# Performance work log

Hardware: AMD Instinct MI355X
Metric: run time of the kernel (lower is better)

Reference implementation:

```python
import jax, jax.numpy as jnp
import numpy as np

NUM_SENT, SENT_LEN, HIDDEN, OUT = 128, 64, 512, 512
N = NUM_SENT * SENT_LEN


def setup_inputs() -> dict:
    key = jax.random.key(0)
    ks = jax.random.split(key, 14)
    s = 1.0 / np.sqrt(HIDDEN)
    so = 1.0 / np.sqrt(OUT)
    return {
        "x": jax.random.normal(ks[0], (NUM_SENT, SENT_LEN, HIDDEN), jnp.float32),
        "mask": jax.random.uniform(ks[1], (N,), jnp.float32),
        "a_ud": jax.random.normal(ks[2], (N, N), jnp.float32) * 0.01,
        "a_lr": jax.random.normal(ks[3], (N, N), jnp.float32) * 0.01,
        "W": jax.random.uniform(ks[4], (OUT, HIDDEN), jnp.float32, -s, s),
        "b": jax.random.uniform(ks[5], (OUT,), jnp.float32, -s, s),
        "W_ud": jax.random.uniform(ks[6], (OUT, HIDDEN), jnp.float32, -s, s),
        "b_ud": jax.random.uniform(ks[7], (OUT,), jnp.float32, -s, s),
        "W_lr": jax.random.uniform(ks[8], (OUT, HIDDEN), jnp.float32, -s, s),
        "b_lr": jax.random.uniform(ks[9], (OUT,), jnp.float32, -s, s),
        "W_g": jax.random.uniform(ks[10], (OUT, HIDDEN), jnp.float32, -s, s),
        "b_g": jax.random.uniform(ks[11], (OUT,), jnp.float32, -s, s),
        "W_go": jax.random.uniform(ks[12], (OUT, OUT), jnp.float32, -so, so),
        "b_go": jax.random.uniform(ks[13], (OUT,), jnp.float32, -so, so),
    }


def reference(x, mask, a_ud, a_lr, W, b, W_ud, b_ud, W_lr, b_lr, W_g, b_g, W_go, b_go):
    num_sent, sent_len, hidden = x.shape
    xf = x.reshape(-1, hidden)                       # [N, H]
    h_ud = a_ud @ xf                                 # [N, H] neighbor aggregation (up/down)
    h_lr = a_lr @ xf                                 # [N, H] neighbor aggregation (left/right)
    h = (xf @ W.T + b) + (h_ud @ W_ud.T + b_ud) + (h_lr @ W_lr.T + b_lr)  # [N, OUT]
    # global node branch: masked mean-pool of relu(linear_g(x))
    n = mask.sum()
    h_g = (mask[None, :] @ jax.nn.relu(xf @ W_g.T + b_g)) / n  # [1, OUT]
    h = h + (h_g @ W_go.T + b_go)                    # broadcast add over N rows
    h = jax.nn.relu(h).reshape(num_sent, sent_len, -1)
    return (h, h_g)
```

## Files before the change

### kernel.cpp

```cpp
#include <hip/hip_runtime.h>
#include <stdint.h>


typedef __attribute__((ext_vector_type(8))) short short8;
typedef __attribute__((ext_vector_type(4))) float f32x4;

typedef const __attribute__((address_space(1))) void* gas1_t;
typedef __attribute__((address_space(3))) void* las3_t;

__device__ __forceinline__ void gload16(const void* g, void* l) {
  __builtin_amdgcn_global_load_lds((gas1_t)g, (las3_t)l, 16, 0, 0);
}

__device__ __forceinline__ unsigned pack2t(float lo, float hi) {
  return __builtin_amdgcn_perm(__float_as_uint(hi), __float_as_uint(lo), 0x07060302u);
}

__device__ __forceinline__ unsigned f2bf_rne(float f) {
  unsigned u = __float_as_uint(f);
  return (u + 0x7FFFu + ((u >> 16) & 1u)) >> 16;
}
__device__ __forceinline__ unsigned pack2_rne(float lo, float hi) {
  return f2bf_rne(lo) | (f2bf_rne(hi) << 16);
}

__global__ __launch_bounds__(256) void k1_convert(
    const float* __restrict__ x, const float* __restrict__ W,
    const float* __restrict__ W_ud, const float* __restrict__ W_lr,
    const float* __restrict__ W_g,
    uint16_t* __restrict__ xb, uint16_t* __restrict__ Yt, uint16_t* __restrict__ Wb1)
{
  unsigned tid = blockIdx.x * 256u + threadIdx.x;
  const float* src;
  uint16_t* dst;
  if (tid < 524288u) {
    src = x + (size_t)tid * 8;
    dst = xb + (size_t)tid * 8;
  } else {
    unsigned r = tid - 524288u;
    unsigned which = r >> 15;
    unsigned e8 = (r & 32767u) * 8;
    src = (which == 0 ? W : which == 1 ? W_ud : which == 2 ? W_lr : W_g) + e8;
    if (which == 0) {
      unsigned n = e8 >> 9, k = e8 & 511u;
      dst = Yt + (size_t)n * 16896 + 16384 + k;
    } else {
      dst = Wb1 + (size_t)(which - 1) * 262144 + e8;
    }
  }
  float4 v0 = ((const float4*)src)[0];
  float4 v1 = ((const float4*)src)[1];
  uint4 p;
  p.x = pack2_rne(v0.x, v0.y); p.y = pack2_rne(v0.z, v0.w);
  p.z = pack2_rne(v1.x, v1.y); p.w = pack2_rne(v1.z, v1.w);
  *(uint4*)dst = p;
}

__global__ __launch_bounds__(256) void k2_gemm1(
    const uint16_t* __restrict__ xb, const uint16_t* __restrict__ Wb1,
    const float* __restrict__ mask, const float* __restrict__ b_g,
    uint16_t* __restrict__ Yt, float* __restrict__ colsum)
{
  __shared__ __align__(16) char smem[34816];
  char* const bufA = smem;
  char* const bufB = smem + 8192;

  const int t = threadIdx.x;
  const int i0 = blockIdx.x * 128;
  const int bn = blockIdx.y;
  const int n0 = bn * 128;
  const int lane = t & 63, w = t >> 6;
  const int q = lane >> 4, l15 = lane & 15;
  const int wm = w >> 1, wn = w & 1;
  const int srow = t >> 2, spart = t & 3;

  f32x4 acc[4][4] = {};

  const uint16_t* const aA0 = xb + (size_t)(i0 + srow) * 512 + spart * 8;
  const uint16_t* const aA1 = aA0 + (size_t)64 * 512;
  const uint16_t* const aB0 = Wb1 + (size_t)(n0 + srow) * 512 + spart * 8;
  const uint16_t* const aB1 = aB0 + (size_t)64 * 512;

  for (int s = 0; s < 16; ++s) {
    __syncthreads();
    const int kk = s << 5;
    gload16(aA0 + kk, bufA + t * 16);
    gload16(aA1 + kk, bufA + 4096 + t * 16);
    gload16(aB0 + kk, bufB + t * 16);
    gload16(aB1 + kk, bufB + 4096 + t * 16);
    __syncthreads();
    short8 af[4], bf[4];
#pragma unroll
    for (int mi = 0; mi < 4; ++mi)
      af[mi] = *(const short8*)(bufA + (wm * 64 + mi * 16 + l15) * 64 + q * 16);
#pragma unroll
    for (int ni = 0; ni < 4; ++ni)
      bf[ni] = *(const short8*)(bufB + (wn * 64 + ni * 16 + l15) * 64 + q * 16);
#pragma unroll
    for (int mi = 0; mi < 4; ++mi)
#pragma unroll
      for (int ni = 0; ni < 4; ++ni)
        acc[mi][ni] = __builtin_amdgcn_mfma_f32_16x16x32_bf16(af[mi], bf[ni], acc[mi][ni], 0, 0, 0);
  }
  __syncthreads();

  const int g = bn >> 2;
  const int jb = (bn & 3) * 128;

  if (g < 2) {
    uint16_t* T = (uint16_t*)smem;
#pragma unroll
    for (int mi = 0; mi < 4; ++mi) {
#pragma unroll
      for (int ni = 0; ni < 4; ++ni) {
        int jl = wn * 64 + ni * 16 + l15;
#pragma unroll
        for (int r = 0; r < 4; ++r) {
          int il = wm * 64 + mi * 16 + q * 4 + r;
          T[jl * 136 + il] = (uint16_t)f2bf_rne(acc[mi][ni][r]);
        }
      }
    }
    __syncthreads();
    const int jl = t >> 1, half = t & 1;
    uint16_t* dst = Yt + (size_t)(jb + jl) * 16896 + (size_t)g * 8192 + i0 + half * 64;
    const uint16_t* srcT = T + jl * 136 + half * 64;
#pragma unroll
    for (int c = 0; c < 8; ++c)
      *(uint4*)(dst + c * 8) = *(const uint4*)(srcT + c * 8);
  } else {
    float mk[4][4];
#pragma unroll
    for (int mi = 0; mi < 4; ++mi)
#pragma unroll
      for (int r = 0; r < 4; ++r)
        mk[mi][r] = mask[i0 + wm * 64 + mi * 16 + q * 4 + r];
#pragma unroll
    for (int ni = 0; ni < 4; ++ni) {
      const int jl = jb + wn * 64 + ni * 16 + l15;
      const float bg = b_g[jl];
      float p = 0.f;
#pragma unroll
      for (int mi = 0; mi < 4; ++mi)
#pragma unroll
        for (int r = 0; r < 4; ++r)
          p += fmaxf(acc[mi][ni][r] + bg, 0.f) * mk[mi][r];
      p += __shfl_xor(p, 16);
      p += __shfl_xor(p, 32);
      if (q == 0) atomicAdd(&colsum[jl], p);
    }
  }
}

__global__ __launch_bounds__(256) void k4_finalize(
    const float* __restrict__ colsum, const float* __restrict__ mask,
    const float* __restrict__ b, const float* __restrict__ b_ud,
    const float* __restrict__ b_lr, const float* __restrict__ W_go,
    const float* __restrict__ b_go,
    float* __restrict__ row_add, float* __restrict__ out_hg)
{
  __shared__ float red[256];
  __shared__ float hg[512];
  const int t = threadIdx.x;
  float s = 0.f;
  for (int k = t; k < 8192; k += 256) s += mask[k];
  red[t] = s;
  __syncthreads();
  for (int o = 128; o > 0; o >>= 1) {
    if (t < o) red[t] += red[t + o];
    __syncthreads();
  }
  const float n = red[0];
  for (int j = t; j < 512; j += 256) hg[j] = colsum[j] / n;
  __syncthreads();

  const int j0 = blockIdx.x * 64;
  const int jj = j0 + (t >> 2);
  const int seg = t & 3;
  const float4* wrow = (const float4*)(W_go + (size_t)jj * 512 + seg * 128);
  float p = 0.f;
#pragma unroll 4
  for (int c = 0; c < 32; ++c) {
    float4 wv = wrow[c];
    const float* h4 = &hg[seg * 128 + c * 4];
    p += wv.x * h4[0] + wv.y * h4[1] + wv.z * h4[2] + wv.w * h4[3];
  }
  p += __shfl_down(p, 2);
  p += __shfl_down(p, 1);
  if ((t & 3) == 0)
    row_add[jj] = b[jj] + b_ud[jj] + b_lr[jj] + b_go[jj] + p;
  if (t < 64) out_hg[j0 + t] = hg[j0 + t];
}

__global__ __launch_bounds__(256) void k5_gemm_big(
    const float* __restrict__ a_ud, const float* __restrict__ a_lr,
    const float* __restrict__ x, const uint16_t* __restrict__ Yt,
    float* __restrict__ out, float* __restrict__ P1)
{
  __shared__ __align__(16) char smem[51200];
  char* const A0 = smem;
  char* const A1 = smem + 9216;
  char* const B0 = smem + 18432;
  char* const B1 = smem + 34816;

  const int t = threadIdx.x;
  const int i0 = blockIdx.x * 64;
  const int j0 = blockIdx.y * 128;
  const int z  = blockIdx.z;
  const int lane = t & 63;
  const int q = lane >> 4, l15 = lane & 15;
  const int w = t >> 6;
  const int wm = w >> 1, wn = w & 1;

  const int arow = t >> 2, aseg = t & 3;
  const int brow = t >> 3;
  const int bchunk = (t & 7) ^ ((t >> 3) & 7);

  f32x4 acc[2][4] = {};
  const int kbase0 = z * 8448;

  float4 av0, av1, av2, av3;
#define A_SRC(gk) ((gk) < 8192 \
    ? a_ud + (size_t)(i0 + arow) * 8192 + (gk) + aseg * 16 \
    : ((gk) < 16384 \
      ? a_lr + (size_t)(i0 + arow) * 8192 + ((gk) - 8192) + aseg * 16 \
      : x + (size_t)(i0 + arow) * 512 + ((gk) - 16384) + aseg * 16))

  {
    const float* as = A_SRC(kbase0);
    av0 = ((const float4*)as)[0]; av1 = ((const float4*)as)[1];
    av2 = ((const float4*)as)[2]; av3 = ((const float4*)as)[3];
#pragma unroll
    for (int r = 0; r < 4; ++r) {
      const int jrow = r * 32 + brow;
      gload16(Yt + (size_t)(j0 + jrow) * 16896 + kbase0 + bchunk * 8,
              B0 + r * 4096 + t * 16);
    }
    uint4 p0, p1;
    p0.x = pack2t(av0.x, av0.y); p0.y = pack2t(av0.z, av0.w);
    p0.z = pack2t(av1.x, av1.y); p0.w = pack2t(av1.z, av1.w);
    p1.x = pack2t(av2.x, av2.y); p1.y = pack2t(av2.z, av2.w);
    p1.z = pack2t(av3.x, av3.y); p1.w = pack2t(av3.z, av3.w);
    *(uint4*)(A0 + arow * 144 + aseg * 32) = p0;
    *(uint4*)(A0 + arow * 144 + aseg * 32 + 16) = p1;
  }

  for (int s = 0; s < 132; ++s) {
    __syncthreads();
    const bool more = (s + 1 < 132);
    char* const cA = (s & 1) ? A1 : A0;
    char* const cB = (s & 1) ? B1 : B0;
    char* const nA = (s & 1) ? A0 : A1;
    char* const nB = (s & 1) ? B0 : B1;

    if (more) {
      const int gk = kbase0 + (s + 1) * 64;
      const float* as = A_SRC(gk);
      av0 = ((const float4*)as)[0]; av1 = ((const float4*)as)[1];
      av2 = ((const float4*)as)[2]; av3 = ((const float4*)as)[3];
#pragma unroll
      for (int r = 0; r < 4; ++r) {
        const int jrow = r * 32 + brow;
        gload16(Yt + (size_t)(j0 + jrow) * 16896 + gk + bchunk * 8,
                nB + r * 4096 + t * 16);
      }
    }

#pragma unroll
    for (int u = 0; u < 2; ++u) {
      const int c = u * 4 + q;
      const int r0 = wm * 32 + l15;
      short8 af0 = *(const short8*)(cA + r0 * 144 + c * 16);
      short8 af1 = *(const short8*)(cA + (r0 + 16) * 144 + c * 16);
      short8 bfr[4];
#pragma unroll
      for (int ni = 0; ni < 4; ++ni) {
        const int jbr = wn * 64 + ni * 16 + l15;
        bfr[ni] = *(const short8*)(cB + jbr * 128 + (c ^ (jbr & 7)) * 16);
      }
#pragma unroll
      for (int ni = 0; ni < 4; ++ni) {
        acc[0][ni] = __builtin_amdgcn_mfma_f32_16x16x32_bf16(af0, bfr[ni], acc[0][ni], 0, 0, 0);
        acc[1][ni] = __builtin_amdgcn_mfma_f32_16x16x32_bf16(af1, bfr[ni], acc[1][ni], 0, 0, 0);
      }
    }

    if (more) {
      uint4 p0, p1;
      p0.x = pack2t(av0.x, av0.y); p0.y = pack2t(av0.z, av0.w);
      p0.z = pack2t(av1.x, av1.y); p0.w = pack2t(av1.z, av1.w);
      p1.x = pack2t(av2.x, av2.y); p1.y = pack2t(av2.z, av2.w);
      p1.z = pack2t(av3.x, av3.y); p1.w = pack2t(av3.z, av3.w);
      *(uint4*)(nA + arow * 144 + aseg * 32) = p0;
      *(uint4*)(nA + arow * 144 + aseg * 32 + 16) = p1;
    }
  }
#undef A_SRC

  float* dst = z ? P1 : out;
#pragma unroll
  for (int ni = 0; ni < 4; ++ni) {
    const int jl = j0 + wn * 64 + ni * 16 + l15;
#pragma unroll
    for (int mi = 0; mi < 2; ++mi)
#pragma unroll
      for (int r = 0; r < 4; ++r) {
        const int il = i0 + wm * 32 + mi * 16 + q * 4 + r;
        dst[(size_t)il * 512 + jl] = acc[mi][ni][r];
      }
  }
}

__global__ __launch_bounds__(256) void k6_combine(
    const float* __restrict__ P1, const float* __restrict__ row_add,
    float* __restrict__ out)
{
  const int idx = blockIdx.x * 256 + threadIdx.x;
  const float4 a = ((const float4*)out)[idx];
  const float4 p = ((const float4*)P1)[idx];
  const float4 r = ((const float4*)row_add)[idx & 127];
  float4 o;
  o.x = fmaxf(a.x + p.x + r.x, 0.f);
  o.y = fmaxf(a.y + p.y + r.y, 0.f);
  o.z = fmaxf(a.z + p.z + r.z, 0.f);
  o.w = fmaxf(a.w + p.w + r.w, 0.f);
  ((float4*)out)[idx] = o;
}

extern "C" void kernel_launch(void* const* d_in, const int* in_sizes, int n_in,
                              void* d_out, int out_size, void* d_ws, size_t ws_size,
                              hipStream_t stream) {
  (void)in_sizes; (void)n_in; (void)out_size; (void)ws_size;
  const float* x    = (const float*)d_in[0];
  const float* mask = (const float*)d_in[1];
  const float* a_ud = (const float*)d_in[2];
  const float* a_lr = (const float*)d_in[3];
  const float* W    = (const float*)d_in[4];
  const float* b    = (const float*)d_in[5];
  const float* W_ud = (const float*)d_in[6];
  const float* b_ud = (const float*)d_in[7];
  const float* W_lr = (const float*)d_in[8];
  const float* b_lr = (const float*)d_in[9];
  const float* W_g  = (const float*)d_in[10];
  const float* b_g  = (const float*)d_in[11];
  const float* W_go = (const float*)d_in[12];
  const float* b_go = (const float*)d_in[13];
  float* out = (float*)d_out;

  char* ws = (char*)d_ws;
  uint16_t* xb     = (uint16_t*)(ws);
  uint16_t* Yt     = (uint16_t*)(ws + 8388608);
  uint16_t* Wb1    = (uint16_t*)(ws + 25690112);
  float*    colsum = (float*)(ws + 27262976);
  float*    rowadd = (float*)(ws + 27265024);
  float*    P1     = (float*)(ws + 27267072);

  hipMemsetAsync(colsum, 0, 512 * sizeof(float), stream);
  k1_convert<<<2560, 256, 0, stream>>>(x, W, W_ud, W_lr, W_g, xb, Yt, Wb1);
  k2_gemm1<<<dim3(64, 12), 256, 0, stream>>>(xb, Wb1, mask, b_g, Yt, colsum);
  k4_finalize<<<8, 256, 0, stream>>>(colsum, mask, b, b_ud, b_lr, W_go, b_go,
                                     rowadd, out + 4194304);
  k5_gemm_big<<<dim3(128, 4, 2), 256, 0, stream>>>(a_ud, a_lr, x, Yt, out, P1);
  k6_combine<<<4096, 256, 0, stream>>>(P1, rowadd, out);
}
```

Before: 902.0 us.

## Retile big GEMM to 128x128 tiles with K=32 steps and configurable split-K

The big fused GEMM now uses 128x128 output tiles (4x4 MFMA per wave) with a K-step of 32 instead of 64x128 tiles with K=64. Shared memory shrinks so more blocks can be resident, with a launch-bounds occupancy hint. Split-K becomes configurable: 4 partitions when the workspace is large enough, otherwise 2, and the combine kernel sums a variable number of partials. The aim is to reuse each A tile across more outputs, cutting re-reads of the fp32 adjacency matrices, and to raise parallelism. The cost is more barriers per unit of work and extra partial-sum traffic.

```diff
diff --git a/kernel.cpp b/kernel.cpp
--- a/kernel.cpp
+++ b/kernel.cpp
@@ -192,19 +192,19 @@
   if (t < 64) out_hg[j0 + t] = hg[j0 + t];
 }
 
-__global__ __launch_bounds__(256) void k5_gemm_big(
+__global__ __launch_bounds__(256, 4) void k5_gemm_big(
     const float* __restrict__ a_ud, const float* __restrict__ a_lr,
     const float* __restrict__ x, const uint16_t* __restrict__ Yt,
-    float* __restrict__ out, float* __restrict__ P1)
-{
-  __shared__ __align__(16) char smem[51200];
+    float* __restrict__ out, float* __restrict__ P, int nsteps)
+{
+  __shared__ __align__(16) char smem[34816];
   char* const A0 = smem;
   char* const A1 = smem + 9216;
   char* const B0 = smem + 18432;
-  char* const B1 = smem + 34816;
+  char* const B1 = smem + 26624;
 
   const int t = threadIdx.x;
-  const int i0 = blockIdx.x * 64;
+  const int i0 = blockIdx.x * 128;
   const int j0 = blockIdx.y * 128;
   const int z  = blockIdx.z;
   const int lane = t & 63;
@@ -212,78 +212,70 @@
   const int w = t >> 6;
   const int wm = w >> 1, wn = w & 1;
 
-  const int arow = t >> 2, aseg = t & 3;
-  const int brow = t >> 3;
-  const int bchunk = (t & 7) ^ ((t >> 3) & 7);
-
-  f32x4 acc[2][4] = {};
-  const int kbase0 = z * 8448;
+  const int arow = t >> 1, ahalf = t & 1;
+  const int brow = t >> 2;
+  const int bchunk = (t & 3) ^ ((t >> 3) & 3);
+
+  f32x4 acc[4][4] = {};
+  const int kbase0 = z * (nsteps << 5);
 
   float4 av0, av1, av2, av3;
 #define A_SRC(gk) ((gk) < 8192 \
-    ? a_ud + (size_t)(i0 + arow) * 8192 + (gk) + aseg * 16 \
+    ? a_ud + (size_t)(i0 + arow) * 8192 + (gk) + ahalf * 16 \
     : ((gk) < 16384 \
-      ? a_lr + (size_t)(i0 + arow) * 8192 + ((gk) - 8192) + aseg * 16 \
-      : x + (size_t)(i0 + arow) * 512 + ((gk) - 16384) + aseg * 16))
+      ? a_lr + (size_t)(i0 + arow) * 8192 + ((gk) - 8192) + ahalf * 16 \
+      : x + (size_t)(i0 + arow) * 512 + ((gk) - 16384) + ahalf * 16))
 
   {
     const float* as = A_SRC(kbase0);
     av0 = ((const float4*)as)[0]; av1 = ((const float4*)as)[1];
     av2 = ((const float4*)as)[2]; av3 = ((const float4*)as)[3];
 #pragma unroll
-    for (int r = 0; r < 4; ++r) {
-      const int jrow = r * 32 + brow;
-      gload16(Yt + (size_t)(j0 + jrow) * 16896 + kbase0 + bchunk * 8,
+    for (int r = 0; r < 2; ++r)
+      gload16(Yt + (size_t)(j0 + brow + r * 64) * 16896 + kbase0 + bchunk * 8,
               B0 + r * 4096 + t * 16);
-    }
     uint4 p0, p1;
     p0.x = pack2t(av0.x, av0.y); p0.y = pack2t(av0.z, av0.w);
     p0.z = pack2t(av1.x, av1.y); p0.w = pack2t(av1.z, av1.w);
     p1.x = pack2t(av2.x, av2.y); p1.y = pack2t(av2.z, av2.w);
     p1.z = pack2t(av3.x, av3.y); p1.w = pack2t(av3.z, av3.w);
-    *(uint4*)(A0 + arow * 144 + aseg * 32) = p0;
-    *(uint4*)(A0 + arow * 144 + aseg * 32 + 16) = p1;
-  }
-
-  for (int s = 0; s < 132; ++s) {
-    __syncthreads();
-    const bool more = (s + 1 < 132);
+    *(uint4*)(A0 + arow * 72 + ahalf * 32) = p0;
+    *(uint4*)(A0 + arow * 72 + ahalf * 32 + 16) = p1;
+  }
+
+  for (int s = 0; s < nsteps; ++s) {
+    __syncthreads();
+    const bool more = (s + 1 < nsteps);
     char* const cA = (s & 1) ? A1 : A0;
     char* const cB = (s & 1) ? B1 : B0;
     char* const nA = (s & 1) ? A0 : A1;
     char* const nB = (s & 1) ? B0 : B1;
 
     if (more) {
-      const int gk = kbase0 + (s + 1) * 64;
+      const int gk = kbase0 + ((s + 1) << 5);
       const float* as = A_SRC(gk);
       av0 = ((const float4*)as)[0]; av1 = ((const float4*)as)[1];
       av2 = ((const float4*)as)[2]; av3 = ((const float4*)as)[3];
 #pragma unroll
-      for (int r = 0; r < 4; ++r) {
-        const int jrow = r * 32 + brow;
-        gload16(Yt + (size_t)(j0 + jrow) * 16896 + gk + bchunk * 8,
+      for (int r = 0; r < 2; ++r)
+        gload16(Yt + (size_t)(j0 + brow + r * 64) * 16896 + gk + bchunk * 8,
                 nB + r * 4096 + t * 16);
-      }
-    }
-
-#pragma unroll
-    for (int u = 0; u < 2; ++u) {
-      const int c = u * 4 + q;
-      const int r0 = wm * 32 + l15;
-      short8 af0 = *(const short8*)(cA + r0 * 144 + c * 16);
-      short8 af1 = *(const short8*)(cA + (r0 + 16) * 144 + c * 16);
-      short8 bfr[4];
-#pragma unroll
-      for (int ni = 0; ni < 4; ++ni) {
-        const int jbr = wn * 64 + ni * 16 + l15;
-        bfr[ni] = *(const short8*)(cB + jbr * 128 + (c ^ (jbr & 7)) * 16);
-      }
-#pragma unroll
-      for (int ni = 0; ni < 4; ++ni) {
-        acc[0][ni] = __builtin_amdgcn_mfma_f32_16x16x32_bf16(af0, bfr[ni], acc[0][ni], 0, 0, 0);
-        acc[1][ni] = __builtin_amdgcn_mfma_f32_16x16x32_bf16(af1, bfr[ni], acc[1][ni], 0, 0, 0);
-      }
-    }
+    }
+
+    short8 af[4], bf[4];
+#pragma unroll
+    for (int mi = 0; mi < 4; ++mi)
+      af[mi] = *(const short8*)(cA + (wm * 64 + mi * 16 + l15) * 72 + q * 16);
+#pragma unroll
+    for (int ni = 0; ni < 4; ++ni) {
+      const int j = wn * 64 + ni * 16 + l15;
+      bf[ni] = *(const short8*)(cB + j * 64 + ((q ^ ((j >> 1) & 3)) * 16));
+    }
+#pragma unroll
+    for (int mi = 0; mi < 4; ++mi)
+#pragma unroll
+      for (int ni = 0; ni < 4; ++ni)
+        acc[mi][ni] = __builtin_amdgcn_mfma_f32_16x16x32_bf16(af[mi], bf[ni], acc[mi][ni], 0, 0, 0);
 
     if (more) {
       uint4 p0, p1;
@@ -291,46 +283,49 @@
       p0.z = pack2t(av1.x, av1.y); p0.w = pack2t(av1.z, av1.w);
       p1.x = pack2t(av2.x, av2.y); p1.y = pack2t(av2.z, av2.w);
       p1.z = pack2t(av3.x, av3.y); p1.w = pack2t(av3.z, av3.w);
-      *(uint4*)(nA + arow * 144 + aseg * 32) = p0;
-      *(uint4*)(nA + arow * 144 + aseg * 32 + 16) = p1;
+      *(uint4*)(nA + arow * 72 + ahalf * 32) = p0;
+      *(uint4*)(nA + arow * 72 + ahalf * 32 + 16) = p1;
     }
   }
 #undef A_SRC
 
-  float* dst = z ? P1 : out;
+  float* dst = z ? P + (size_t)(z - 1) * 4194304 : out;
 #pragma unroll
   for (int ni = 0; ni < 4; ++ni) {
     const int jl = j0 + wn * 64 + ni * 16 + l15;
 #pragma unroll
-    for (int mi = 0; mi < 2; ++mi)
+    for (int mi = 0; mi < 4; ++mi)
 #pragma unroll
       for (int r = 0; r < 4; ++r) {
-        const int il = i0 + wm * 32 + mi * 16 + q * 4 + r;
+        const int il = i0 + wm * 64 + mi * 16 + q * 4 + r;
         dst[(size_t)il * 512 + jl] = acc[mi][ni][r];
       }
   }
 }
 
 __global__ __launch_bounds__(256) void k6_combine(
-    const float* __restrict__ P1, const float* __restrict__ row_add,
-    float* __restrict__ out)
+    const float* __restrict__ P, const float* __restrict__ row_add,
+    float* __restrict__ out, int npart)
 {
   const int idx = blockIdx.x * 256 + threadIdx.x;
-  const float4 a = ((const float4*)out)[idx];
-  const float4 p = ((const float4*)P1)[idx];
+  float4 a = ((const float4*)out)[idx];
+  for (int p = 0; p < npart; ++p) {
+    const float4 v = ((const float4*)P)[(size_t)p * 1048576 + idx];
+    a.x += v.x; a.y += v.y; a.z += v.z; a.w += v.w;
+  }
   const float4 r = ((const float4*)row_add)[idx & 127];
   float4 o;
-  o.x = fmaxf(a.x + p.x + r.x, 0.f);
-  o.y = fmaxf(a.y + p.y + r.y, 0.f);
-  o.z = fmaxf(a.z + p.z + r.z, 0.f);
-  o.w = fmaxf(a.w + p.w + r.w, 0.f);
+  o.x = fmaxf(a.x + r.x, 0.f);
+  o.y = fmaxf(a.y + r.y, 0.f);
+  o.z = fmaxf(a.z + r.z, 0.f);
+  o.w = fmaxf(a.w + r.w, 0.f);
   ((float4*)out)[idx] = o;
 }
 
 extern "C" void kernel_launch(void* const* d_in, const int* in_sizes, int n_in,
                               void* d_out, int out_size, void* d_ws, size_t ws_size,
                               hipStream_t stream) {
-  (void)in_sizes; (void)n_in; (void)out_size; (void)ws_size;
+  (void)in_sizes; (void)n_in; (void)out_size;
   const float* x    = (const float*)d_in[0];
   const float* mask = (const float*)d_in[1];
   const float* a_ud = (const float*)d_in[2];
@@ -353,13 +348,16 @@
   uint16_t* Wb1    = (uint16_t*)(ws + 25690112);
   float*    colsum = (float*)(ws + 27262976);
   float*    rowadd = (float*)(ws + 27265024);
-  float*    P1     = (float*)(ws + 27267072);
+  float*    P      = (float*)(ws + 27267072);
+
+  const int Z = (ws_size >= 77598720u) ? 4 : 2;
+  const int nsteps = (16896 / Z) / 32;
 
   hipMemsetAsync(colsum, 0, 512 * sizeof(float), stream);
   k1_convert<<<2560, 256, 0, stream>>>(x, W, W_ud, W_lr, W_g, xb, Yt, Wb1);
   k2_gemm1<<<dim3(64, 12), 256, 0, stream>>>(xb, Wb1, mask, b_g, Yt, colsum);
   k4_finalize<<<8, 256, 0, stream>>>(colsum, mask, b, b_ud, b_lr, W_go, b_go,
                                      rowadd, out + 4194304);
-  k5_gemm_big<<<dim3(128, 4, 2), 256, 0, stream>>>(a_ud, a_lr, x, Yt, out, P1);
-  k6_combine<<<4096, 256, 0, stream>>>(P1, rowadd, out);
-}
+  k5_gemm_big<<<dim3(64, 4, Z), 256, 0, stream>>>(a_ud, a_lr, x, Yt, out, P, nsteps);
+  k6_combine<<<4096, 256, 0, stream>>>(P, rowadd, out, Z - 1);
+}
```

Result: faster. 863.9 us (-4.2%).
